# Optimization experiments

Measured on AMD Instinct MI355X. Metric: run time of the kernel, lower is better.

## Reference

```python
import jax, jax.numpy as jnp
import numpy as np
from jax import lax

INPUT_SIZE = 3
HIDDEN = 32
SEQ = 24
BATCH = 131072
FC1 = 16


def setup_inputs() -> dict:
    key = jax.random.key(0)
    ks = jax.random.split(key, 9)
    s_ih = 1.0 / np.sqrt(HIDDEN)
    # PyTorch LSTM params: weight_ih (4H, input), weight_hh (4H, H), biases (4H,)
    return {
        "x": jax.random.normal(ks[0], (BATCH, SEQ, INPUT_SIZE), dtype=jnp.float32),
        "w_ih": jax.random.uniform(ks[1], (4 * HIDDEN, INPUT_SIZE), minval=-s_ih, maxval=s_ih, dtype=jnp.float32),
        "w_hh": jax.random.uniform(ks[2], (4 * HIDDEN, HIDDEN), minval=-s_ih, maxval=s_ih, dtype=jnp.float32),
        "b_ih": jax.random.uniform(ks[3], (4 * HIDDEN,), minval=-s_ih, maxval=s_ih, dtype=jnp.float32),
        "b_hh": jax.random.uniform(ks[4], (4 * HIDDEN,), minval=-s_ih, maxval=s_ih, dtype=jnp.float32),
        "w1": jax.random.uniform(ks[5], (FC1, HIDDEN), minval=-s_ih, maxval=s_ih, dtype=jnp.float32),
        "b1": jax.random.uniform(ks[6], (FC1,), minval=-s_ih, maxval=s_ih, dtype=jnp.float32),
        "w2": jax.random.uniform(ks[7], (1, FC1), minval=-0.25, maxval=0.25, dtype=jnp.float32),
        "b2": jax.random.uniform(ks[8], (1,), minval=-0.25, maxval=0.25, dtype=jnp.float32),
    }


def reference(x, w_ih, w_hh, b_ih, b_hh, w1, b1, w2, b2):
    B = x.shape[0]
    b = b_ih + b_hh  # fuse the two bias vectors

    def step(carry, xt):
        h, c = carry
        # gates: (B, 4H) in PyTorch order [i, f, g, o]
        gates = xt @ w_ih.T + h @ w_hh.T + b
        i, f, g, o = jnp.split(gates, 4, axis=-1)
        c_new = jax.nn.sigmoid(f) * c + jax.nn.sigmoid(i) * jnp.tanh(g)
        h_new = jax.nn.sigmoid(o) * jnp.tanh(c_new)
        return (h_new, c_new), None

    h0 = jnp.zeros((B, HIDDEN), dtype=x.dtype)
    c0 = jnp.zeros((B, HIDDEN), dtype=x.dtype)
    xs = jnp.transpose(x, (1, 0, 2))  # (T, B, F)
    (h_last, _), _ = lax.scan(step, (h0, c0), xs)

    # Head: Linear(H,16) -> ReLU -> Dropout(identity in eval) -> Linear(16,1)
    hid = jax.nn.relu(h_last @ w1.T + b1)
    logit = hid @ w2.T + b2  # (B, 1)
    return logit
```

## Files before the change

### kernel.cpp

```cpp
#include <hip/hip_runtime.h>


typedef _Float16 f16x8 __attribute__((ext_vector_type(8)));
typedef _Float16 f16x4 __attribute__((ext_vector_type(4)));
typedef _Float16 f16x2 __attribute__((ext_vector_type(2)));
typedef float f32x4 __attribute__((ext_vector_type(4)));
typedef float f32x2 __attribute__((ext_vector_type(2)));

#define L2E 1.4426950408889634f

#if __has_builtin(__builtin_amdgcn_mfma_f32_16x16x16f16)
#define HAVE_MFMA16 1
#else
#define HAVE_MFMA16 0
#endif

__device__ __forceinline__ float fexp2(float v) { return __builtin_amdgcn_exp2f(v); }
__device__ __forceinline__ float frcp(float v)  { return __builtin_amdgcn_rcpf(v); }

__global__ __launch_bounds__(256, 2)
void lstm_fused(const float* __restrict__ x,
                const float* __restrict__ w_ih,
                const float* __restrict__ w_hh,
                const float* __restrict__ b_ih,
                const float* __restrict__ b_hh,
                const float* __restrict__ w1,
                const float* __restrict__ b1,
                const float* __restrict__ w2,
                const float* __restrict__ b2,
                float* __restrict__ out)
{
    __shared__ int2  xq[24 * 128];
    __shared__ float w1s[512];
    __shared__ float b1s[16];
    __shared__ float w2s[16];
    __shared__ float b2s;

    const int tid  = threadIdx.x;
    const int lane = tid & 63;
    const int wv   = tid >> 6;
    const int c    = lane & 15;
    const int g    = lane >> 4;
    const int blockBase = blockIdx.x * 128;

    for (int i = tid; i < 512; i += 256) w1s[i] = w1[i];
    if (tid < 16) { b1s[tid] = b1[tid]; w2s[tid] = w2[tid]; }
    if (tid == 16) b2s = b2[0];

    for (int it = 0; it < 12; ++it) {
        int p = tid + it * 256;
        int n = p / 24;
        int t = p - n * 24;
        const float* xp = x + ((blockBase + n) * 24 + t) * 3;
        union { f16x4 h; int2 i2; } tq;
        tq.h[0] = (_Float16)xp[0];
        tq.h[1] = (_Float16)xp[1];
        tq.h[2] = (_Float16)xp[2];
        tq.h[3] = (_Float16)1.0f;
        xq[t * 128 + n] = tq.i2;
    }

    f16x8 whh[8];
#if HAVE_MFMA16
    f16x4 wib[8];
#else
    f16x8 wib[8];
#endif
    const int ubase = 8 * (c >> 2) + (c & 3);
#pragma unroll
    for (int G = 0; G < 4; ++G) {
        const float scale = (G == 2) ? (2.f * L2E) : L2E;
#pragma unroll
        for (int p = 0; p < 2; ++p) {
            const int row = G * 32 + ubase + 4 * p;
            const float* wr = w_hh + row * 32 + g * 8;
            f16x8 a;
#pragma unroll
            for (int e = 0; e < 8; ++e) a[e] = (_Float16)(wr[e] * scale);
            whh[G * 2 + p] = a;
            _Float16 c0 = 0, c1 = 0, c2 = 0, c3 = 0;
            if (g == 0) {
                c0 = (_Float16)(w_ih[row * 3 + 0] * scale);
                c1 = (_Float16)(w_ih[row * 3 + 1] * scale);
                c2 = (_Float16)(w_ih[row * 3 + 2] * scale);
                c3 = (_Float16)((b_ih[row] + b_hh[row]) * scale);
            }
#if HAVE_MFMA16
            f16x4 bb = {c0, c1, c2, c3};
#else
            f16x8 bb = {c0, c1, c2, c3, 0, 0, 0, 0};
#endif
            wib[G * 2 + p] = bb;
        }
    }

    __syncthreads();

    f32x2 cz = {0.f, 0.f};
    f32x2 cst2[8];
#pragma unroll
    for (int q = 0; q < 8; ++q) cst2[q] = cz;
    union hu_t { f16x2 p2[4]; f16x8 v; int4 i4; } hreg[2];
    hreg[0].i4 = make_int4(0, 0, 0, 0);
    hreg[1].i4 = make_int4(0, 0, 0, 0);

    const int n0 = wv * 16 + c;
    int2 xv[2];
    xv[0] = xq[n0];
    xv[1] = xq[n0 + 64];

#pragma unroll 1
    for (int t = 0; t < 24; ++t) {
        const int tn = (t < 23) ? t + 1 : 23;
        int2 xn0 = xq[tn * 128 + n0];
        int2 xn1 = xq[tn * 128 + n0 + 64];

        f32x4 acc[2][2][4];
        const f32x4 z = {0.f, 0.f, 0.f, 0.f};
#pragma unroll
        for (int s = 0; s < 2; ++s) {
            f16x8 hf = hreg[s].v;
#pragma unroll
            for (int p = 0; p < 2; ++p) {
#pragma unroll
                for (int G = 0; G < 4; ++G)
                    acc[s][p][G] = __builtin_amdgcn_mfma_f32_16x16x32_f16(
                        whh[2 * G + p], hf, z, 0, 0, 0);
            }
        }
#pragma unroll
        for (int s = 0; s < 2; ++s) {
            int xlo = (g == 0) ? xv[s].x : 0;
            int xhi = (g == 0) ? xv[s].y : 0;
#if HAVE_MFMA16
            union { int2 i2; f16x4 v; } xu;
            xu.i2 = make_int2(xlo, xhi);
            f16x4 xf = xu.v;
#else
            union { int4 i4; f16x8 v; } xu;
            xu.i4 = make_int4(xlo, xhi, 0, 0);
            f16x8 xf = xu.v;
#endif
#pragma unroll
            for (int p = 0; p < 2; ++p) {
#pragma unroll
                for (int G = 0; G < 4; ++G)
#if HAVE_MFMA16
                    acc[s][p][G] = __builtin_amdgcn_mfma_f32_16x16x16f16(
                        wib[2 * G + p], xf, acc[s][p][G], 0, 0, 0);
#else
                    acc[s][p][G] = __builtin_amdgcn_mfma_f32_16x16x32_f16(
                        wib[2 * G + p], xf, acc[s][p][G], 0, 0, 0);
#endif
            }
        }

        f32x2 vi[8], vf[8], vg[8], vo[8];
#pragma unroll
        for (int q = 0; q < 8; ++q) {
            const int s = q >> 2, p = (q >> 1) & 1, j = q & 1;
            vi[q][0] = acc[s][p][0][2 * j]; vi[q][1] = acc[s][p][0][2 * j + 1];
            vf[q][0] = acc[s][p][1][2 * j]; vf[q][1] = acc[s][p][1][2 * j + 1];
            vg[q][0] = acc[s][p][2][2 * j]; vg[q][1] = acc[s][p][2][2 * j + 1];
            vo[q][0] = acc[s][p][3][2 * j]; vo[q][1] = acc[s][p][3][2 * j + 1];
        }
        f32x2 ex[8], ey[8], ef[8];
#pragma unroll
        for (int q = 0; q < 8; ++q) {
            ex[q][0] = fexp2(-vi[q][0]); ex[q][1] = fexp2(-vi[q][1]);
            ey[q][0] = fexp2(vg[q][0]);  ey[q][1] = fexp2(vg[q][1]);
            ef[q][0] = fexp2(-vf[q][0]); ef[q][1] = fexp2(-vf[q][1]);
        }
        const f32x2 one = {1.f, 1.f};
        const f32x2 K2  = {2.f * L2E, 2.f * L2E};
        f32x2 axy[8], efp[8], r1[8];
#pragma unroll
        for (int q = 0; q < 8; ++q) {
            axy[q] = (one + ex[q]) * (one + ey[q]);
            efp[q] = one + ef[q];
            f32x2 dd = axy[q] * efp[q];
            r1[q][0] = frcp(dd[0]); r1[q][1] = frcp(dd[1]);
        }
        f32x2 ez[8], ew[8];
#pragma unroll
        for (int q = 0; q < 8; ++q) {
            f32x2 igs = (ey[q] * K2 - K2) * efp[q] * r1[q];
            f32x2 fs  = axy[q] * r1[q];
            cst2[q] = fs * cst2[q] + igs;
            ew[q][0] = fexp2(-vo[q][0]); ew[q][1] = fexp2(-vo[q][1]);
            ez[q][0] = fexp2(cst2[q][0]); ez[q][1] = fexp2(cst2[q][1]);
        }
#pragma unroll
        for (int q = 0; q < 8; ++q) {
            const int s = q >> 2, p = (q >> 1) & 1, j = q & 1;
            f32x2 d2 = (one + ew[q]) * (one + ez[q]);
            f32x2 r2; r2[0] = frcp(d2[0]); r2[1] = frcp(d2[1]);
            f32x2 hn = (ez[q] - one) * r2;
            f16x2 hh; hh[0] = (_Float16)hn[0]; hh[1] = (_Float16)hn[1];
            hreg[s].p2[2 * p + j] = hh;
        }
        xv[0] = xn0;
        xv[1] = xn1;
    }

#pragma unroll
    for (int s = 0; s < 2; ++s) {
        float hfin[8];
#pragma unroll
        for (int d = 0; d < 8; ++d) hfin[d] = (float)hreg[s].v[d];
        float hid[16];
#pragma unroll
        for (int q = 0; q < 16; ++q) {
            const float4* wrow = (const float4*)(w1s + q * 32 + g * 8);
            float4 wa = wrow[0], wb = wrow[1];
            float sm = wa.x * hfin[0] + wa.y * hfin[1] + wa.z * hfin[2] + wa.w * hfin[3]
                     + wb.x * hfin[4] + wb.y * hfin[5] + wb.z * hfin[6] + wb.w * hfin[7];
            sm += __shfl_xor(sm, 16);
            sm += __shfl_xor(sm, 32);
            hid[q] = sm;
        }
        float po = b2s;
#pragma unroll
        for (int q = 0; q < 16; ++q)
            po = fmaf(fmaxf(hid[q] + b1s[q], 0.f), w2s[q], po);
        if (g == 0) out[blockBase + s * 64 + n0] = po;
    }
}

extern "C" void kernel_launch(void* const* d_in, const int* in_sizes, int n_in,
                              void* d_out, int out_size, void* d_ws, size_t ws_size,
                              hipStream_t stream) {
    (void)in_sizes; (void)n_in; (void)d_ws; (void)ws_size; (void)out_size;
    const float* x    = (const float*)d_in[0];
    const float* w_ih = (const float*)d_in[1];
    const float* w_hh = (const float*)d_in[2];
    const float* b_ih = (const float*)d_in[3];
    const float* b_hh = (const float*)d_in[4];
    const float* w1   = (const float*)d_in[5];
    const float* b1   = (const float*)d_in[6];
    const float* w2   = (const float*)d_in[7];
    const float* b2   = (const float*)d_in[8];
    float* outp = (float*)d_out;

    dim3 grid(131072 / 128);
    dim3 block(256);
    hipLaunchKernelGGL(lstm_fused, grid, block, 0, stream,
                       x, w_ih, w_hh, b_ih, b_hh, w1, b1, w2, b2, outp);
}
```

Before: 95.60 us.

## Halve per-wave batch tile and raise occupancy to four blocks per CU

```diff
diff --git a/kernel.cpp b/kernel.cpp
--- a/kernel.cpp
+++ b/kernel.cpp
@@ -18,7 +18,7 @@
 __device__ __forceinline__ float fexp2(float v) { return __builtin_amdgcn_exp2f(v); }
 __device__ __forceinline__ float frcp(float v)  { return __builtin_amdgcn_rcpf(v); }
 
-__global__ __launch_bounds__(256, 2)
+__global__ __launch_bounds__(256, 4)
 void lstm_fused(const float* __restrict__ x,
                 const float* __restrict__ w_ih,
                 const float* __restrict__ w_hh,
@@ -30,7 +30,7 @@
                 const float* __restrict__ b2,
                 float* __restrict__ out)
 {
-    __shared__ int2  xq[24 * 128];
+    __shared__ int2  xq[24 * 64];
     __shared__ float w1s[512];
     __shared__ float b1s[16];
     __shared__ float w2s[16];
@@ -41,13 +41,13 @@
     const int wv   = tid >> 6;
     const int c    = lane & 15;
     const int g    = lane >> 4;
-    const int blockBase = blockIdx.x * 128;
+    const int blockBase = blockIdx.x * 64;
 
     for (int i = tid; i < 512; i += 256) w1s[i] = w1[i];
     if (tid < 16) { b1s[tid] = b1[tid]; w2s[tid] = w2[tid]; }
     if (tid == 16) b2s = b2[0];
 
-    for (int it = 0; it < 12; ++it) {
+    for (int it = 0; it < 6; ++it) {
         int p = tid + it * 256;
         int n = p / 24;
         int t = p - n * 24;
@@ -57,7 +57,7 @@
         tq.h[1] = (_Float16)xp[1];
         tq.h[2] = (_Float16)xp[2];
         tq.h[3] = (_Float16)1.0f;
-        xq[t * 128 + n] = tq.i2;
+        xq[t * 64 + n] = tq.i2;
     }
 
     f16x8 whh[8];
@@ -97,41 +97,30 @@
     __syncthreads();
 
     f32x2 cz = {0.f, 0.f};
-    f32x2 cst2[8];
-#pragma unroll
-    for (int q = 0; q < 8; ++q) cst2[q] = cz;
-    union hu_t { f16x2 p2[4]; f16x8 v; int4 i4; } hreg[2];
-    hreg[0].i4 = make_int4(0, 0, 0, 0);
-    hreg[1].i4 = make_int4(0, 0, 0, 0);
+    f32x2 cst2[4] = {cz, cz, cz, cz};
+    union hu_t { f16x2 p2[4]; f16x8 v; int4 i4; } hreg;
+    hreg.i4 = make_int4(0, 0, 0, 0);
 
     const int n0 = wv * 16 + c;
-    int2 xv[2];
-    xv[0] = xq[n0];
-    xv[1] = xq[n0 + 64];
+    int2 xv = xq[n0];
 
 #pragma unroll 1
     for (int t = 0; t < 24; ++t) {
         const int tn = (t < 23) ? t + 1 : 23;
-        int2 xn0 = xq[tn * 128 + n0];
-        int2 xn1 = xq[tn * 128 + n0 + 64];
-
-        f32x4 acc[2][2][4];
+        int2 xnxt = xq[tn * 64 + n0];
+
+        f32x4 acc[2][4];
         const f32x4 z = {0.f, 0.f, 0.f, 0.f};
-#pragma unroll
-        for (int s = 0; s < 2; ++s) {
-            f16x8 hf = hreg[s].v;
-#pragma unroll
-            for (int p = 0; p < 2; ++p) {
-#pragma unroll
-                for (int G = 0; G < 4; ++G)
-                    acc[s][p][G] = __builtin_amdgcn_mfma_f32_16x16x32_f16(
-                        whh[2 * G + p], hf, z, 0, 0, 0);
-            }
-        }
-#pragma unroll
-        for (int s = 0; s < 2; ++s) {
-            int xlo = (g == 0) ? xv[s].x : 0;
-            int xhi = (g == 0) ? xv[s].y : 0;
+        f16x8 hf = hreg.v;
+#pragma unroll
+        for (int p = 0; p < 2; ++p)
+#pragma unroll
+            for (int G = 0; G < 4; ++G)
+                acc[p][G] = __builtin_amdgcn_mfma_f32_16x16x32_f16(
+                    whh[2 * G + p], hf, z, 0, 0, 0);
+        {
+            int xlo = (g == 0) ? xv.x : 0;
+            int xhi = (g == 0) ? xv.y : 0;
 #if HAVE_MFMA16
             union { int2 i2; f16x4 v; } xu;
             xu.i2 = make_int2(xlo, xhi);
@@ -142,89 +131,81 @@
             f16x8 xf = xu.v;
 #endif
 #pragma unroll
-            for (int p = 0; p < 2; ++p) {
+            for (int p = 0; p < 2; ++p)
 #pragma unroll
                 for (int G = 0; G < 4; ++G)
 #if HAVE_MFMA16
-                    acc[s][p][G] = __builtin_amdgcn_mfma_f32_16x16x16f16(
-                        wib[2 * G + p], xf, acc[s][p][G], 0, 0, 0);
-#else
-                    acc[s][p][G] = __builtin_amdgcn_mfma_f32_16x16x32_f16(
-                        wib[2 * G + p], xf, acc[s][p][G], 0, 0, 0);
-#endif
-            }
-        }
-
-        f32x2 vi[8], vf[8], vg[8], vo[8];
-#pragma unroll
-        for (int q = 0; q < 8; ++q) {
-            const int s = q >> 2, p = (q >> 1) & 1, j = q & 1;
-            vi[q][0] = acc[s][p][0][2 * j]; vi[q][1] = acc[s][p][0][2 * j + 1];
-            vf[q][0] = acc[s][p][1][2 * j]; vf[q][1] = acc[s][p][1][2 * j + 1];
-            vg[q][0] = acc[s][p][2][2 * j]; vg[q][1] = acc[s][p][2][2 * j + 1];
-            vo[q][0] = acc[s][p][3][2 * j]; vo[q][1] = acc[s][p][3][2 * j + 1];
-        }
-        f32x2 ex[8], ey[8], ef[8];
-#pragma unroll
-        for (int q = 0; q < 8; ++q) {
-            ex[q][0] = fexp2(-vi[q][0]); ex[q][1] = fexp2(-vi[q][1]);
-            ey[q][0] = fexp2(vg[q][0]);  ey[q][1] = fexp2(vg[q][1]);
-            ef[q][0] = fexp2(-vf[q][0]); ef[q][1] = fexp2(-vf[q][1]);
+                    acc[p][G] = __builtin_amdgcn_mfma_f32_16x16x16f16(
+                        wib[2 * G + p], xf, acc[p][G], 0, 0, 0);
+#else
+                    acc[p][G] = __builtin_amdgcn_mfma_f32_16x16x32_f16(
+                        wib[2 * G + p], xf, acc[p][G], 0, 0, 0);
+#endif
+        }
+
+        f32x2 ew[4];
+#pragma unroll
+        for (int q = 0; q < 4; ++q) {
+            const int p = q >> 1, j = q & 1;
+            ew[q][0] = fexp2(-acc[p][3][2 * j]);
+            ew[q][1] = fexp2(-acc[p][3][2 * j + 1]);
+        }
+        f32x2 ex[4], ey[4], ef[4];
+#pragma unroll
+        for (int q = 0; q < 4; ++q) {
+            const int p = q >> 1, j = q & 1;
+            ex[q][0] = fexp2(-acc[p][0][2 * j]); ex[q][1] = fexp2(-acc[p][0][2 * j + 1]);
+            ey[q][0] = fexp2( acc[p][2][2 * j]); ey[q][1] = fexp2( acc[p][2][2 * j + 1]);
+            ef[q][0] = fexp2(-acc[p][1][2 * j]); ef[q][1] = fexp2(-acc[p][1][2 * j + 1]);
         }
         const f32x2 one = {1.f, 1.f};
         const f32x2 K2  = {2.f * L2E, 2.f * L2E};
-        f32x2 axy[8], efp[8], r1[8];
-#pragma unroll
-        for (int q = 0; q < 8; ++q) {
+        f32x2 axy[4], efp[4], r1[4];
+#pragma unroll
+        for (int q = 0; q < 4; ++q) {
             axy[q] = (one + ex[q]) * (one + ey[q]);
             efp[q] = one + ef[q];
             f32x2 dd = axy[q] * efp[q];
             r1[q][0] = frcp(dd[0]); r1[q][1] = frcp(dd[1]);
         }
-        f32x2 ez[8], ew[8];
-#pragma unroll
-        for (int q = 0; q < 8; ++q) {
+        f32x2 ez[4];
+#pragma unroll
+        for (int q = 0; q < 4; ++q) {
             f32x2 igs = (ey[q] * K2 - K2) * efp[q] * r1[q];
             f32x2 fs  = axy[q] * r1[q];
             cst2[q] = fs * cst2[q] + igs;
-            ew[q][0] = fexp2(-vo[q][0]); ew[q][1] = fexp2(-vo[q][1]);
             ez[q][0] = fexp2(cst2[q][0]); ez[q][1] = fexp2(cst2[q][1]);
         }
 #pragma unroll
-        for (int q = 0; q < 8; ++q) {
-            const int s = q >> 2, p = (q >> 1) & 1, j = q & 1;
+        for (int q = 0; q < 4; ++q) {
             f32x2 d2 = (one + ew[q]) * (one + ez[q]);
             f32x2 r2; r2[0] = frcp(d2[0]); r2[1] = frcp(d2[1]);
             f32x2 hn = (ez[q] - one) * r2;
             f16x2 hh; hh[0] = (_Float16)hn[0]; hh[1] = (_Float16)hn[1];
-            hreg[s].p2[2 * p + j] = hh;
-        }
-        xv[0] = xn0;
-        xv[1] = xn1;
-    }
-
-#pragma unroll
-    for (int s = 0; s < 2; ++s) {
-        float hfin[8];
-#pragma unroll
-        for (int d = 0; d < 8; ++d) hfin[d] = (float)hreg[s].v[d];
-        float hid[16];
-#pragma unroll
-        for (int q = 0; q < 16; ++q) {
-            const float4* wrow = (const float4*)(w1s + q * 32 + g * 8);
-            float4 wa = wrow[0], wb = wrow[1];
-            float sm = wa.x * hfin[0] + wa.y * hfin[1] + wa.z * hfin[2] + wa.w * hfin[3]
-                     + wb.x * hfin[4] + wb.y * hfin[5] + wb.z * hfin[6] + wb.w * hfin[7];
-            sm += __shfl_xor(sm, 16);
-            sm += __shfl_xor(sm, 32);
-            hid[q] = sm;
-        }
-        float po = b2s;
-#pragma unroll
-        for (int q = 0; q < 16; ++q)
-            po = fmaf(fmaxf(hid[q] + b1s[q], 0.f), w2s[q], po);
-        if (g == 0) out[blockBase + s * 64 + n0] = po;
-    }
+            hreg.p2[q] = hh;
+        }
+        xv = xnxt;
+    }
+
+    float hfin[8];
+#pragma unroll
+    for (int d = 0; d < 8; ++d) hfin[d] = (float)hreg.v[d];
+    float hid[16];
+#pragma unroll
+    for (int q = 0; q < 16; ++q) {
+        const float4* wrow = (const float4*)(w1s + q * 32 + g * 8);
+        float4 wa = wrow[0], wb = wrow[1];
+        float sm = wa.x * hfin[0] + wa.y * hfin[1] + wa.z * hfin[2] + wa.w * hfin[3]
+                 + wb.x * hfin[4] + wb.y * hfin[5] + wb.z * hfin[6] + wb.w * hfin[7];
+        sm += __shfl_xor(sm, 16);
+        sm += __shfl_xor(sm, 32);
+        hid[q] = sm;
+    }
+    float po = b2s;
+#pragma unroll
+    for (int q = 0; q < 16; ++q)
+        po = fmaf(fmaxf(hid[q] + b1s[q], 0.f), w2s[q], po);
+    if (g == 0) out[blockBase + n0] = po;
 }
 
 extern "C" void kernel_launch(void* const* d_in, const int* in_sizes, int n_in,
@@ -242,7 +223,7 @@
     const float* b2   = (const float*)d_in[8];
     float* outp = (float*)d_out;
 
-    dim3 grid(131072 / 128);
+    dim3 grid(131072 / 64);
     dim3 block(256);
     hipLaunchKernelGGL(lstm_fused, grid, block, 0, stream,
                        x, w_ih, w_hh, b_ih, b_hh, w1, b1, w2, b2, outp);
```

Result: no change. 97.42 us (+1.9%).
